# Performance work log

Measured on AMD Instinct MI355X. Metric: run time of the kernel, lower is better.

The kernel has to match this reference:

```python
import jax, jax.numpy as jnp
import numpy as np

N = 16384   # nodes
E = 524288  # edges (avg degree 32)
D = 32      # input_dim == output_dim


def setup_inputs() -> dict:
    key = jax.random.key(0)
    k_x, k_e, k_wa, k_ba, k_wu, k_bu = jax.random.split(key, 6)
    x = jax.random.normal(k_x, (N, D), dtype=jnp.float32)
    edge_index = jax.random.randint(k_e, (2, E), 0, N, dtype=jnp.int32)
    # nn.Linear init: U(-1/sqrt(fan_in), 1/sqrt(fan_in)), weight shape [out, in]
    bound = 1.0 / np.sqrt(D)
    W_agg = jax.random.uniform(k_wa, (D, D), jnp.float32, -bound, bound)
    b_agg = jax.random.uniform(k_ba, (D,), jnp.float32, -bound, bound)
    W_upd = jax.random.uniform(k_wu, (D, D), jnp.float32, -bound, bound)
    b_upd = jax.random.uniform(k_bu, (D,), jnp.float32, -bound, bound)
    return {"x": x, "edge_index": edge_index, "W_agg": W_agg, "b_agg": b_agg,
            "W_upd": W_upd, "b_upd": b_upd}


def reference(x, edge_index, W_agg, b_agg, W_upd, b_upd):
    n = x.shape[0]
    src, dst = edge_index[0], edge_index[1]
    # Dense symmetric 0/1 adjacency, exactly as the torch module builds it
    # (duplicate edges still write 1 via .set, matching index_put semantics).
    adj = jnp.zeros((n, n), dtype=x.dtype)
    adj = adj.at[src, dst].set(1.0)
    adj = adj.at[dst, src].set(1.0)
    messages = adj @ x                              # [N, D]
    aggregated = messages @ W_agg.T + b_agg         # aggregate_fn(messages)
    updated = x @ W_upd.T + b_upd + aggregated      # update_fn(x) + aggregated
    return updated
```

## Files before the change

### kernel.cpp

```cpp
#include <hip/hip_runtime.h>

#define D 32
#define CAP 384


__global__ void gnn_edge_bits(const int* __restrict__ src,
                              const int* __restrict__ dst,
                              unsigned int* __restrict__ bm,
                              int E, int wpr) {
    int e = blockIdx.x * blockDim.x + threadIdx.x;
    if (e >= E) return;
    int s = src[e];
    int d = dst[e];
    atomicOr(&bm[(size_t)d * wpr + (s >> 5)], 1u << (s & 31));
    atomicOr(&bm[(size_t)s * wpr + (d >> 5)], 1u << (d & 31));
}

__global__ __launch_bounds__(256) void gnn_gather_update(
        const unsigned int* __restrict__ bm,
        const float* __restrict__ x,
        float* __restrict__ out,
        const float* __restrict__ W_agg,
        const float* __restrict__ b_agg,
        const float* __restrict__ W_upd,
        const float* __restrict__ b_upd,
        int wpr) {
    __shared__ float sWa[D][D + 1];
    __shared__ float sWu[D][D + 1];
    __shared__ float sb[D];
    __shared__ float sx[4][D];
    __shared__ float sm[4][D];
    __shared__ int   slist[4][CAP];

    int t = threadIdx.x;
    for (int i = t; i < D * D; i += 256) {
        sWa[i >> 5][i & 31] = W_agg[i];
        sWu[i >> 5][i & 31] = W_upd[i];
    }
    if (t < D) sb[t] = b_agg[t] + b_upd[t];

    int lane = t & 63;
    int wv   = t >> 6;
    int dim  = lane & 31;
    int half = lane >> 5;
    size_t node = (size_t)blockIdx.x * 4 + wv;

    if (lane < D) sx[wv][lane] = x[node * D + lane];

    const unsigned int* row = bm + node * (size_t)wpr;
    unsigned int wb[8];
#pragma unroll
    for (int c = 0; c < 8; ++c) wb[c] = row[c * 64 + lane];

    int myc = 0;
#pragma unroll
    for (int c = 0; c < 8; ++c) myc += __popc(wb[c]);

    int pre = myc;
#pragma unroll
    for (int off = 1; off < 64; off <<= 1) {
        int v = __shfl_up(pre, off, 64);
        if (lane >= off) pre += v;
    }
    int total = __shfl(pre, 63, 64);
    pre -= myc;

    if (total <= CAP) {
        int p = pre;
#pragma unroll
        for (int c = 0; c < 8; ++c) {
            unsigned int ww = wb[c];
            int base = (c * 64 + lane) * 32;
            while (ww) {
                int b = __ffs(ww) - 1;
                ww &= ww - 1;
                slist[wv][p++] = base + b;
            }
        }
    }
    __syncthreads();

    float acc = 0.f;
    if (total <= CAP) {
        int j = half;
        for (; j + 8 <= total; j += 8) {
            int c0 = slist[wv][j + 0];
            int c1 = slist[wv][j + 2];
            int c2 = slist[wv][j + 4];
            int c3 = slist[wv][j + 6];
            float v0 = x[(size_t)c0 * D + dim];
            float v1 = x[(size_t)c1 * D + dim];
            float v2 = x[(size_t)c2 * D + dim];
            float v3 = x[(size_t)c3 * D + dim];
            acc += v0; acc += v1; acc += v2; acc += v3;
        }
        for (; j < total; j += 2)
            acc += x[(size_t)slist[wv][j] * D + dim];
        acc += __shfl_xor(acc, 32, 64);
    } else {
        for (int c = 0; c < 8; ++c) {
            unsigned long long m = __ballot(wb[c] != 0);
            while (m) {
                int l = __ffsll(m) - 1;
                m &= m - 1;
                unsigned int ww = __shfl(wb[c], l, 64);
                int basecol = (c * 64 + l) * 32;
                while (ww) {
                    int b = __ffs(ww) - 1;
                    ww &= ww - 1;
                    acc += x[(size_t)(basecol + b) * D + dim];
                }
            }
        }
    }
    if (lane < D) sm[wv][lane] = acc;
    __syncthreads();

    if (t < 128) {
        int ns = t >> 5;
        int o  = t & 31;
        float r = sb[o];
#pragma unroll
        for (int k = 0; k < D; ++k)
            r += sx[ns][k] * sWu[o][k] + sm[ns][k] * sWa[o][k];
        out[((size_t)blockIdx.x * 4 + ns) * D + o] = r;
    }
}

#define HASH_BITS 20
#define HASH_SIZE (1u << HASH_BITS)
#define EMPTY_KEY 0xFFFFFFFFu

__global__ void gnn_edge_scatter(const int* __restrict__ src,
                                 const int* __restrict__ dst,
                                 const float* __restrict__ x,
                                 float* __restrict__ msg,
                                 unsigned int* __restrict__ htab,
                                 int E) {
    int e = blockIdx.x * blockDim.x + threadIdx.x;
    if (e >= E) return;
    int s = src[e];
    int d = dst[e];
    int a = s < d ? s : d;
    int b = s < d ? d : s;
    unsigned int key = ((unsigned int)a << 14) | (unsigned int)b;
    unsigned int h = (key * 2654435761u) >> (32 - HASH_BITS);
    bool inserted;
    for (;;) {
        unsigned int prev = atomicCAS(&htab[h], EMPTY_KEY, key);
        if (prev == EMPTY_KEY) { inserted = true; break; }
        if (prev == key)       { inserted = false; break; }
        h = (h + 1) & (HASH_SIZE - 1);
    }
    if (!inserted) return;
    const float* xs = x + (size_t)s * D;
    const float* xd = x + (size_t)d * D;
    if (s == d) {
        float* mrow = msg + (size_t)s * D;
#pragma unroll
        for (int i = 0; i < D; ++i) atomicAdd(&mrow[i], xs[i]);
    } else {
        float* ms = msg + (size_t)s * D;
        float* md = msg + (size_t)d * D;
#pragma unroll
        for (int i = 0; i < D; ++i) {
            atomicAdd(&ms[i], xd[i]);
            atomicAdd(&md[i], xs[i]);
        }
    }
}

__global__ __launch_bounds__(256) void gnn_update(
        const float* __restrict__ x,
        float* __restrict__ out,
        const float* __restrict__ W_agg,
        const float* __restrict__ b_agg,
        const float* __restrict__ W_upd,
        const float* __restrict__ b_upd) {
    __shared__ float sWa[D][D + 1];
    __shared__ float sWu[D][D + 1];
    __shared__ float sb[D];
    __shared__ float sx[8][D];
    __shared__ float sm[8][D];
    int t = threadIdx.x;
    for (int i = t; i < D * D; i += 256) {
        sWa[i >> 5][i & 31] = W_agg[i];
        sWu[i >> 5][i & 31] = W_upd[i];
    }
    if (t < D) sb[t] = b_agg[t] + b_upd[t];
    int g = t >> 5, o = t & 31;
    size_t node = (size_t)blockIdx.x * 8 + g;
    sx[g][o] = x[node * D + o];
    sm[g][o] = out[node * D + o];
    __syncthreads();
    float acc = sb[o];
#pragma unroll
    for (int k = 0; k < D; ++k) {
        acc += sx[g][k] * sWu[o][k];
        acc += sm[g][k] * sWa[o][k];
    }
    out[node * D + o] = acc;
}


extern "C" void kernel_launch(void* const* d_in, const int* in_sizes, int n_in,
                              void* d_out, int out_size, void* d_ws, size_t ws_size,
                              hipStream_t stream) {
    const float* x      = (const float*)d_in[0];
    const int*   eidx   = (const int*)d_in[1];
    const float* W_agg  = (const float*)d_in[2];
    const float* b_agg  = (const float*)d_in[3];
    const float* W_upd  = (const float*)d_in[4];
    const float* b_upd  = (const float*)d_in[5];
    float* out = (float*)d_out;

    const int E = in_sizes[1] / 2;
    const int N = in_sizes[0] / D;
    const int* src = eidx;
    const int* dst = eidx + E;

    const int wpr = N >> 5;
    const size_t bm_bytes = (size_t)N * wpr * sizeof(unsigned int);

    if (ws_size >= bm_bytes) {
        unsigned int* bm = (unsigned int*)d_ws;
        hipMemsetAsync(bm, 0, bm_bytes, stream);
        gnn_edge_bits<<<(E + 255) / 256, 256, 0, stream>>>(src, dst, bm, E, wpr);
        gnn_gather_update<<<N / 4, 256, 0, stream>>>(bm, x, out, W_agg, b_agg,
                                                     W_upd, b_upd, wpr);
    } else {
        unsigned int* htab = (unsigned int*)d_ws;
        hipMemsetAsync(out, 0, (size_t)N * D * sizeof(float), stream);
        hipMemsetAsync(htab, 0xFF, (size_t)HASH_SIZE * sizeof(unsigned int), stream);
        gnn_edge_scatter<<<(E + 255) / 256, 256, 0, stream>>>(src, dst, x, out, htab, E);
        gnn_update<<<N / 8, 256, 0, stream>>>(x, out, W_agg, b_agg, W_upd, b_upd);
    }
}
```

Before: 134.9 us.

## Replace dense adjacency bitmap with per-node neighbor lists and LDS dedup

Stops building a 32 MB dense adjacency bitmap (memset plus atomicOr) and instead appends each edge endpoint into a fixed-capacity per-node list using padded atomic counters. The gather kernel then reads only the node's list, deduplicates neighbors with a per-wave shared-memory bitmap and atomicOr, compacts the unique indices, and sums x rows. This cuts the memset and the bitmap scan traffic. In exchange it adds contended atomicAdd on counters during build and an overflow fallback that scans all edges for high-degree nodes. The fallback could be very slow if a node's degree ever exceeds the cap.

```diff
diff --git a/kernel.cpp b/kernel.cpp
--- a/kernel.cpp
+++ b/kernel.cpp
@@ -1,36 +1,42 @@
 #include <hip/hip_runtime.h>
 
 #define D 32
-#define CAP 384
-
-
-__global__ void gnn_edge_bits(const int* __restrict__ src,
+#define CAP 256
+#define CSTRIDE 16
+
+__global__ void gnn_csr_build(const int* __restrict__ src,
                               const int* __restrict__ dst,
-                              unsigned int* __restrict__ bm,
-                              int E, int wpr) {
+                              int* __restrict__ cnt,
+                              int* __restrict__ list, int E) {
     int e = blockIdx.x * blockDim.x + threadIdx.x;
     if (e >= E) return;
     int s = src[e];
     int d = dst[e];
-    atomicOr(&bm[(size_t)d * wpr + (s >> 5)], 1u << (s & 31));
-    atomicOr(&bm[(size_t)s * wpr + (d >> 5)], 1u << (d & 31));
+    int p = atomicAdd(&cnt[(size_t)d * CSTRIDE], 1);
+    if (p < CAP) list[(size_t)d * CAP + p] = s;
+    int q = atomicAdd(&cnt[(size_t)s * CSTRIDE], 1);
+    if (q < CAP) list[(size_t)s * CAP + q] = d;
 }
 
 __global__ __launch_bounds__(256) void gnn_gather_update(
-        const unsigned int* __restrict__ bm,
+        const int* __restrict__ cnt,
+        const int* __restrict__ list,
+        const int* __restrict__ src,
+        const int* __restrict__ dst,
+        int E,
         const float* __restrict__ x,
         float* __restrict__ out,
         const float* __restrict__ W_agg,
         const float* __restrict__ b_agg,
         const float* __restrict__ W_upd,
-        const float* __restrict__ b_upd,
-        int wpr) {
+        const float* __restrict__ b_upd) {
     __shared__ float sWa[D][D + 1];
     __shared__ float sWu[D][D + 1];
     __shared__ float sb[D];
     __shared__ float sx[4][D];
     __shared__ float sm[4][D];
-    __shared__ int   slist[4][CAP];
+    __shared__ unsigned int sbit[4][512];
+    __shared__ int slist[4][64];
 
     int t = threadIdx.x;
     for (int i = t; i < D * D; i += 256) {
@@ -47,72 +53,74 @@
 
     if (lane < D) sx[wv][lane] = x[node * D + lane];
 
-    const unsigned int* row = bm + node * (size_t)wpr;
-    unsigned int wb[8];
-#pragma unroll
-    for (int c = 0; c < 8; ++c) wb[c] = row[c * 64 + lane];
-
-    int myc = 0;
-#pragma unroll
-    for (int c = 0; c < 8; ++c) myc += __popc(wb[c]);
-
-    int pre = myc;
-#pragma unroll
-    for (int off = 1; off < 64; off <<= 1) {
-        int v = __shfl_up(pre, off, 64);
-        if (lane >= off) pre += v;
-    }
-    int total = __shfl(pre, 63, 64);
-    pre -= myc;
-
-    if (total <= CAP) {
-        int p = pre;
-#pragma unroll
-        for (int c = 0; c < 8; ++c) {
-            unsigned int ww = wb[c];
-            int base = (c * 64 + lane) * 32;
-            while (ww) {
-                int b = __ffs(ww) - 1;
-                ww &= ww - 1;
-                slist[wv][p++] = base + b;
-            }
+#pragma unroll
+    for (int i = 0; i < 8; ++i) sbit[wv][i * 64 + lane] = 0u;
+
+    int deg = cnt[node * CSTRIDE];
+    float acc = 0.f;
+
+    if (deg <= CAP) {
+        const int* ml = list + node * CAP;
+        for (int base = 0; base < deg; base += 64) {
+            int idx = -1, keep = 0;
+            if (base + lane < deg) {
+                idx = ml[base + lane];
+                unsigned int old = atomicOr(&sbit[wv][idx >> 5], 1u << (idx & 31));
+                keep = !((old >> (idx & 31)) & 1u);
+            }
+            int pre = keep;
+#pragma unroll
+            for (int off = 1; off < 64; off <<= 1) {
+                int v = __shfl_up(pre, off, 64);
+                if (lane >= off) pre += v;
+            }
+            int ckn = __shfl(pre, 63, 64);
+            if (keep) slist[wv][pre - 1] = idx;
+            __asm__ __volatile__("s_waitcnt lgkmcnt(0)" ::: "memory");
+
+            int j = half;
+            for (; j + 8 <= ckn; j += 8) {
+                int c0 = slist[wv][j + 0];
+                int c1 = slist[wv][j + 2];
+                int c2 = slist[wv][j + 4];
+                int c3 = slist[wv][j + 6];
+                float v0 = x[(size_t)c0 * D + dim];
+                float v1 = x[(size_t)c1 * D + dim];
+                float v2 = x[(size_t)c2 * D + dim];
+                float v3 = x[(size_t)c3 * D + dim];
+                acc += v0; acc += v1; acc += v2; acc += v3;
+            }
+            for (; j < ckn; j += 2)
+                acc += x[(size_t)slist[wv][j] * D + dim];
         }
-    }
-    __syncthreads();
-
-    float acc = 0.f;
-    if (total <= CAP) {
-        int j = half;
-        for (; j + 8 <= total; j += 8) {
-            int c0 = slist[wv][j + 0];
-            int c1 = slist[wv][j + 2];
-            int c2 = slist[wv][j + 4];
-            int c3 = slist[wv][j + 6];
-            float v0 = x[(size_t)c0 * D + dim];
-            float v1 = x[(size_t)c1 * D + dim];
-            float v2 = x[(size_t)c2 * D + dim];
-            float v3 = x[(size_t)c3 * D + dim];
-            acc += v0; acc += v1; acc += v2; acc += v3;
+    } else {
+        for (int base = 0; base < E; base += 64) {
+            int e = base + lane;
+            int nbr = -1, keep = 0;
+            if (e < E) {
+                int s = src[e], d = dst[e];
+                if (s == (int)node)      nbr = d;
+                else if (d == (int)node) nbr = s;
+            }
+            if (nbr >= 0) {
+                unsigned int old = atomicOr(&sbit[wv][nbr >> 5], 1u << (nbr & 31));
+                keep = !((old >> (nbr & 31)) & 1u);
+            }
+            int pre = keep;
+#pragma unroll
+            for (int off = 1; off < 64; off <<= 1) {
+                int v = __shfl_up(pre, off, 64);
+                if (lane >= off) pre += v;
+            }
+            int ckn = __shfl(pre, 63, 64);
+            if (keep) slist[wv][pre - 1] = nbr;
+            __asm__ __volatile__("s_waitcnt lgkmcnt(0)" ::: "memory");
+            for (int j = half; j < ckn; j += 2)
+                acc += x[(size_t)slist[wv][j] * D + dim];
         }
-        for (; j < total; j += 2)
-            acc += x[(size_t)slist[wv][j] * D + dim];
-        acc += __shfl_xor(acc, 32, 64);
-    } else {
-        for (int c = 0; c < 8; ++c) {
-            unsigned long long m = __ballot(wb[c] != 0);
-            while (m) {
-                int l = __ffsll(m) - 1;
-                m &= m - 1;
-                unsigned int ww = __shfl(wb[c], l, 64);
-                int basecol = (c * 64 + l) * 32;
-                while (ww) {
-                    int b = __ffs(ww) - 1;
-                    ww &= ww - 1;
-                    acc += x[(size_t)(basecol + b) * D + dim];
-                }
-            }
-        }
-    }
+    }
+
+    acc += __shfl_xor(acc, 32, 64);
     if (lane < D) sm[wv][lane] = acc;
     __syncthreads();
 
@@ -219,15 +227,17 @@
     const int* src = eidx;
     const int* dst = eidx + E;
 
-    const int wpr = N >> 5;
-    const size_t bm_bytes = (size_t)N * wpr * sizeof(unsigned int);
-
-    if (ws_size >= bm_bytes) {
-        unsigned int* bm = (unsigned int*)d_ws;
-        hipMemsetAsync(bm, 0, bm_bytes, stream);
-        gnn_edge_bits<<<(E + 255) / 256, 256, 0, stream>>>(src, dst, bm, E, wpr);
-        gnn_gather_update<<<N / 4, 256, 0, stream>>>(bm, x, out, W_agg, b_agg,
-                                                     W_upd, b_upd, wpr);
+    const size_t cnt_bytes  = (size_t)N * CSTRIDE * sizeof(int);
+    const size_t list_bytes = (size_t)N * CAP * sizeof(int);
+
+    if (ws_size >= cnt_bytes + list_bytes) {
+        int* cnt  = (int*)d_ws;
+        int* list = (int*)((char*)d_ws + cnt_bytes);
+        hipMemsetAsync(cnt, 0, cnt_bytes, stream);
+        gnn_csr_build<<<(E + 255) / 256, 256, 0, stream>>>(src, dst, cnt, list, E);
+        gnn_gather_update<<<N / 4, 256, 0, stream>>>(cnt, list, src, dst, E,
+                                                     x, out, W_agg, b_agg,
+                                                     W_upd, b_upd);
     } else {
         unsigned int* htab = (unsigned int*)d_ws;
         hipMemsetAsync(out, 0, (size_t)N * D * sizeof(float), stream);
```

Result: slower. 153.2 us (+13.5%).

## Replace global adjacency bitmap with two-level edge binning and per-block shared bitmaps

Applied to the files above, without the earlier changes.

Drops the 32 MB global bitmap (memset plus scattered atomicOr plus full-row reads) in favour of two binning passes that bucket packed edge entries by destination node group into global lists. Each gather block then builds a 16-node bitmap in shared memory for deduplication, and gathers and applies the linear layers for those 16 nodes. This cuts global memory traffic, at the cost of two extra kernels, spill-buffer handling and much larger shared memory per block. The hash fallback key is also changed to be N-based.

```diff
diff --git a/kernel.cpp b/kernel.cpp
--- a/kernel.cpp
+++ b/kernel.cpp
@@ -1,129 +1,208 @@
 #include <hip/hip_runtime.h>
 
 #define D 32
-#define CAP 384
-
-
-__global__ void gnn_edge_bits(const int* __restrict__ src,
-                              const int* __restrict__ dst,
-                              unsigned int* __restrict__ bm,
-                              int E, int wpr) {
-    int e = blockIdx.x * blockDim.x + threadIdx.x;
-    if (e >= E) return;
-    int s = src[e];
-    int d = dst[e];
-    atomicOr(&bm[(size_t)d * wpr + (s >> 5)], 1u << (s & 31));
-    atomicOr(&bm[(size_t)s * wpr + (d >> 5)], 1u << (d & 31));
+
+#define NB_C     8
+#define FPERC    128
+#define NB_F     1024
+#define CCAP     524288
+#define FCAP     4096
+#define SPILLCAP 8192
+#define A_EPB    4096
+#define A_CAP    512
+#define A2_EPB   8192
+#define A2_CAP   128
+#define GCAP     256
+
+__global__ __launch_bounds__(256) void gnn_bin_coarse(
+        const int* __restrict__ src, const int* __restrict__ dst, int E,
+        unsigned int* __restrict__ clist, int* __restrict__ ccnt,
+        unsigned int* __restrict__ spill, int* __restrict__ spillcnt) {
+    __shared__ unsigned int buf[4][NB_C][A_CAP];
+    __shared__ int bcnt[4][NB_C];
+    int t = threadIdx.x, wv = t >> 6, lane = t & 63;
+    if (lane < NB_C) bcnt[wv][lane] = 0;
+    __syncthreads();
+
+    int base = blockIdx.x * A_EPB;
+    int lim  = min(base + A_EPB, E);
+    for (int e = base + t; e < lim; e += 256) {
+        int s = src[e], d2 = dst[e];
+        unsigned int e1 = ((unsigned int)d2 << 14) | (unsigned int)s;
+        unsigned int e2 = ((unsigned int)s  << 14) | (unsigned int)d2;
+        int b1 = d2 >> 11, b2 = s >> 11;
+        int p1 = atomicAdd(&bcnt[wv][b1], 1);
+        if (p1 < A_CAP) buf[wv][b1][p1] = e1;
+        else { int sp = atomicAdd(spillcnt, 1); if (sp < SPILLCAP) spill[sp] = e1; }
+        int p2 = atomicAdd(&bcnt[wv][b2], 1);
+        if (p2 < A_CAP) buf[wv][b2][p2] = e2;
+        else { int sp = atomicAdd(spillcnt, 1); if (sp < SPILLCAP) spill[sp] = e2; }
+    }
+    __syncthreads();
+
+    for (int b = 0; b < NB_C; ++b) {
+        int c = bcnt[wv][b]; if (c > A_CAP) c = A_CAP;
+        if (c == 0) continue;
+        int gbase = 0;
+        if (lane == 0) gbase = atomicAdd(&ccnt[b], c);
+        gbase = __shfl(gbase, 0, 64);
+        for (int i = lane; i < c; i += 64) {
+            int pos = gbase + i;
+            unsigned int v = buf[wv][b][i];
+            if (pos < CCAP) clist[(size_t)b * CCAP + pos] = v;
+            else { int sp = atomicAdd(spillcnt, 1); if (sp < SPILLCAP) spill[sp] = v; }
+        }
+    }
+}
+
+__global__ __launch_bounds__(256) void gnn_bin_fine(
+        const unsigned int* __restrict__ clist, const int* __restrict__ ccnt,
+        unsigned int* __restrict__ flist, int* __restrict__ fcnt,
+        unsigned int* __restrict__ spill, int* __restrict__ spillcnt) {
+    int cb = blockIdx.x & (NB_C - 1);
+    int slice = blockIdx.x >> 3;
+    int cnt = ccnt[cb]; if (cnt > CCAP) cnt = CCAP;
+    int base = slice * A2_EPB;
+    if (base >= cnt) return;
+    int lim = min(base + A2_EPB, cnt);
+
+    __shared__ unsigned int buf[FPERC][A2_CAP];
+    __shared__ int bcnt[FPERC];
+    int t = threadIdx.x;
+    if (t < FPERC) bcnt[t] = 0;
+    __syncthreads();
+
+    const unsigned int* cl = clist + (size_t)cb * CCAP;
+    for (int i = base + t; i < lim; i += 256) {
+        unsigned int en = cl[i];
+        int fb = (en >> 18) & (FPERC - 1);
+        int p = atomicAdd(&bcnt[fb], 1);
+        if (p < A2_CAP) buf[fb][p] = en;
+        else { int sp = atomicAdd(spillcnt, 1); if (sp < SPILLCAP) spill[sp] = en; }
+    }
+    __syncthreads();
+
+    if (t < FPERC) {
+        int c = bcnt[t]; if (c > A2_CAP) c = A2_CAP;
+        if (c) {
+            int fg = cb * FPERC + t;
+            int g = atomicAdd(&fcnt[fg], c);
+            unsigned int* fl = flist + (size_t)fg * FCAP;
+            for (int i = 0; i < c; ++i) {
+                int pos = g + i;
+                unsigned int v = buf[t][i];
+                if (pos < FCAP) fl[pos] = v;
+                else { int sp = atomicAdd(spillcnt, 1); if (sp < SPILLCAP) spill[sp] = v; }
+            }
+        }
+    }
 }
 
 __global__ __launch_bounds__(256) void gnn_gather_update(
-        const unsigned int* __restrict__ bm,
-        const float* __restrict__ x,
-        float* __restrict__ out,
-        const float* __restrict__ W_agg,
-        const float* __restrict__ b_agg,
-        const float* __restrict__ W_upd,
-        const float* __restrict__ b_upd,
-        int wpr) {
-    __shared__ float sWa[D][D + 1];
-    __shared__ float sWu[D][D + 1];
-    __shared__ float sb[D];
-    __shared__ float sx[4][D];
-    __shared__ float sm[4][D];
-    __shared__ int   slist[4][CAP];
+        const unsigned int* __restrict__ flist, const int* __restrict__ fcnt,
+        const unsigned int* __restrict__ spill, const int* __restrict__ spillcnt,
+        const float* __restrict__ x, float* __restrict__ out,
+        const float* __restrict__ W_agg, const float* __restrict__ b_agg,
+        const float* __restrict__ W_upd, const float* __restrict__ b_upd) {
+    __shared__ unsigned int sbit[16][512];
+    __shared__ float sWa[D][D + 1], sWu[D][D + 1];
+    __shared__ float sbias[D];
+    __shared__ float sxn[16][D], smsg[16][D];
+    __shared__ int slist[4][GCAP];
 
     int t = threadIdx.x;
+    int fb = blockIdx.x;
+
+    for (int i = t; i < 16 * 512; i += 256) ((unsigned int*)sbit)[i] = 0u;
     for (int i = t; i < D * D; i += 256) {
         sWa[i >> 5][i & 31] = W_agg[i];
         sWu[i >> 5][i & 31] = W_upd[i];
     }
-    if (t < D) sb[t] = b_agg[t] + b_upd[t];
-
-    int lane = t & 63;
-    int wv   = t >> 6;
-    int dim  = lane & 31;
-    int half = lane >> 5;
-    size_t node = (size_t)blockIdx.x * 4 + wv;
-
-    if (lane < D) sx[wv][lane] = x[node * D + lane];
-
-    const unsigned int* row = bm + node * (size_t)wpr;
-    unsigned int wb[8];
-#pragma unroll
-    for (int c = 0; c < 8; ++c) wb[c] = row[c * 64 + lane];
-
-    int myc = 0;
-#pragma unroll
-    for (int c = 0; c < 8; ++c) myc += __popc(wb[c]);
-
-    int pre = myc;
-#pragma unroll
-    for (int off = 1; off < 64; off <<= 1) {
-        int v = __shfl_up(pre, off, 64);
-        if (lane >= off) pre += v;
-    }
-    int total = __shfl(pre, 63, 64);
-    pre -= myc;
-
-    if (total <= CAP) {
-        int p = pre;
-#pragma unroll
-        for (int c = 0; c < 8; ++c) {
-            unsigned int ww = wb[c];
-            int base = (c * 64 + lane) * 32;
-            while (ww) {
-                int b = __ffs(ww) - 1;
-                ww &= ww - 1;
-                slist[wv][p++] = base + b;
+    if (t < D) sbias[t] = b_agg[t] + b_upd[t];
+    for (int i = t; i < 16 * D; i += 256)
+        ((float*)sxn)[i] = x[(size_t)fb * 16 * D + i];
+    __syncthreads();
+
+    int cnt = fcnt[fb]; if (cnt > FCAP) cnt = FCAP;
+    const unsigned int* fl = flist + (size_t)fb * FCAP;
+    for (int i = t; i < cnt; i += 256) {
+        unsigned int en = fl[i];
+        int nl = (en >> 14) & 15;
+        int nbr = en & 16383;
+        atomicOr(&sbit[nl][nbr >> 5], 1u << (nbr & 31));
+    }
+    int sc = *spillcnt; if (sc > SPILLCAP) sc = SPILLCAP;
+    for (int i = t; i < sc; i += 256) {
+        unsigned int en = spill[i];
+        int node = en >> 14;
+        if ((node >> 4) == fb) {
+            int nbr = en & 16383;
+            atomicOr(&sbit[node & 15][nbr >> 5], 1u << (nbr & 31));
+        }
+    }
+    __syncthreads();
+
+    int wv = t >> 6, lane = t & 63, dim = lane & 31, half = lane >> 5;
+    for (int q = 0; q < 4; ++q) {
+        int nl = wv * 4 + q;
+        unsigned int w[8];
+#pragma unroll
+        for (int c = 0; c < 8; ++c) w[c] = sbit[nl][c * 64 + lane];
+        int myc = 0;
+#pragma unroll
+        for (int c = 0; c < 8; ++c) myc += __popc(w[c]);
+        int pre = myc;
+#pragma unroll
+        for (int off = 1; off < 64; off <<= 1) {
+            int v = __shfl_up(pre, off, 64);
+            if (lane >= off) pre += v;
+        }
+        int total = __shfl(pre, 63, 64);
+        pre -= myc;
+        float acc = 0.f;
+        if (total <= GCAP) {
+            int p = pre;
+#pragma unroll
+            for (int c = 0; c < 8; ++c) {
+                unsigned int ww = w[c];
+                int bb = (c * 64 + lane) * 32;
+                while (ww) { int b = __ffs(ww) - 1; ww &= ww - 1; slist[wv][p++] = bb + b; }
             }
-        }
-    }
-    __syncthreads();
-
-    float acc = 0.f;
-    if (total <= CAP) {
-        int j = half;
-        for (; j + 8 <= total; j += 8) {
-            int c0 = slist[wv][j + 0];
-            int c1 = slist[wv][j + 2];
-            int c2 = slist[wv][j + 4];
-            int c3 = slist[wv][j + 6];
-            float v0 = x[(size_t)c0 * D + dim];
-            float v1 = x[(size_t)c1 * D + dim];
-            float v2 = x[(size_t)c2 * D + dim];
-            float v3 = x[(size_t)c3 * D + dim];
-            acc += v0; acc += v1; acc += v2; acc += v3;
-        }
-        for (; j < total; j += 2)
-            acc += x[(size_t)slist[wv][j] * D + dim];
-        acc += __shfl_xor(acc, 32, 64);
-    } else {
-        for (int c = 0; c < 8; ++c) {
-            unsigned long long m = __ballot(wb[c] != 0);
-            while (m) {
-                int l = __ffsll(m) - 1;
-                m &= m - 1;
-                unsigned int ww = __shfl(wb[c], l, 64);
-                int basecol = (c * 64 + l) * 32;
-                while (ww) {
-                    int b = __ffs(ww) - 1;
-                    ww &= ww - 1;
-                    acc += x[(size_t)(basecol + b) * D + dim];
+            int j = half;
+            for (; j + 8 <= total; j += 8) {
+                int c0 = slist[wv][j + 0], c1 = slist[wv][j + 2];
+                int c2 = slist[wv][j + 4], c3 = slist[wv][j + 6];
+                float v0 = x[(size_t)c0 * D + dim];
+                float v1 = x[(size_t)c1 * D + dim];
+                float v2 = x[(size_t)c2 * D + dim];
+                float v3 = x[(size_t)c3 * D + dim];
+                acc += v0; acc += v1; acc += v2; acc += v3;
+            }
+            for (; j < total; j += 2) acc += x[(size_t)slist[wv][j] * D + dim];
+        } else {
+            for (int c = 0; c < 8; ++c) {
+                unsigned long long m = __ballot(w[c] != 0);
+                while (m) {
+                    int l = __ffsll(m) - 1; m &= m - 1;
+                    unsigned int ww = __shfl(w[c], l, 64);
+                    int bb = (c * 64 + l) * 32;
+                    while (ww) { int b = __ffs(ww) - 1; ww &= ww - 1;
+                                 acc += x[(size_t)(bb + b) * D + dim]; }
                 }
             }
         }
-    }
-    if (lane < D) sm[wv][lane] = acc;
-    __syncthreads();
-
-    if (t < 128) {
-        int ns = t >> 5;
-        int o  = t & 31;
-        float r = sb[o];
+        acc += __shfl_xor(acc, 32, 64);
+        if (lane < D) smsg[nl][lane] = acc;
+    }
+    __syncthreads();
+
+    for (int o = t; o < 16 * D; o += 256) {
+        int nl = o >> 5, od = o & 31;
+        float r = sbias[od];
 #pragma unroll
         for (int k = 0; k < D; ++k)
-            r += sx[ns][k] * sWu[o][k] + sm[ns][k] * sWa[o][k];
-        out[((size_t)blockIdx.x * 4 + ns) * D + o] = r;
+            r += sxn[nl][k] * sWu[od][k] + smsg[nl][k] * sWa[od][k];
+        out[((size_t)fb * 16 + nl) * D + od] = r;
     }
 }
 
@@ -135,30 +214,28 @@
                                  const int* __restrict__ dst,
                                  const float* __restrict__ x,
                                  float* __restrict__ msg,
-                                 unsigned int* __restrict__ htab,
-                                 int E) {
+                                 unsigned int* __restrict__ htab, int E, int N) {
     int e = blockIdx.x * blockDim.x + threadIdx.x;
     if (e >= E) return;
-    int s = src[e];
-    int d = dst[e];
-    int a = s < d ? s : d;
-    int b = s < d ? d : s;
-    unsigned int key = ((unsigned int)a << 14) | (unsigned int)b;
-    unsigned int h = (key * 2654435761u) >> (32 - HASH_BITS);
+    int s = src[e], d = dst[e];
+    int a = s < d ? s : d, b = s < d ? d : s;
+    unsigned long long key = (unsigned long long)a * N + b;
+    unsigned int k32 = (unsigned int)(key & 0xFFFFFFFEu) | 1u;
+    unsigned int h = ((unsigned int)key * 2654435761u) >> (32 - HASH_BITS);
     bool inserted;
     for (;;) {
-        unsigned int prev = atomicCAS(&htab[h], EMPTY_KEY, key);
+        unsigned int prev = atomicCAS(&htab[h], EMPTY_KEY, k32);
         if (prev == EMPTY_KEY) { inserted = true; break; }
-        if (prev == key)       { inserted = false; break; }
+        if (prev == k32)       { inserted = false; break; }
         h = (h + 1) & (HASH_SIZE - 1);
     }
     if (!inserted) return;
     const float* xs = x + (size_t)s * D;
     const float* xd = x + (size_t)d * D;
     if (s == d) {
-        float* mrow = msg + (size_t)s * D;
-#pragma unroll
-        for (int i = 0; i < D; ++i) atomicAdd(&mrow[i], xs[i]);
+        float* m = msg + (size_t)s * D;
+#pragma unroll
+        for (int i = 0; i < D; ++i) atomicAdd(&m[i], xs[i]);
     } else {
         float* ms = msg + (size_t)s * D;
         float* md = msg + (size_t)d * D;
@@ -171,17 +248,11 @@
 }
 
 __global__ __launch_bounds__(256) void gnn_update(
-        const float* __restrict__ x,
-        float* __restrict__ out,
-        const float* __restrict__ W_agg,
-        const float* __restrict__ b_agg,
-        const float* __restrict__ W_upd,
-        const float* __restrict__ b_upd) {
-    __shared__ float sWa[D][D + 1];
-    __shared__ float sWu[D][D + 1];
-    __shared__ float sb[D];
-    __shared__ float sx[8][D];
-    __shared__ float sm[8][D];
+        const float* __restrict__ x, float* __restrict__ out,
+        const float* __restrict__ W_agg, const float* __restrict__ b_agg,
+        const float* __restrict__ W_upd, const float* __restrict__ b_upd) {
+    __shared__ float sWa[D][D + 1], sWu[D][D + 1], sb[D];
+    __shared__ float sx[8][D], sm[8][D];
     int t = threadIdx.x;
     for (int i = t; i < D * D; i += 256) {
         sWa[i >> 5][i & 31] = W_agg[i];
@@ -195,10 +266,8 @@
     __syncthreads();
     float acc = sb[o];
 #pragma unroll
-    for (int k = 0; k < D; ++k) {
-        acc += sx[g][k] * sWu[o][k];
-        acc += sm[g][k] * sWa[o][k];
-    }
+    for (int k = 0; k < D; ++k)
+        acc += sx[g][k] * sWu[o][k] + sm[g][k] * sWa[o][k];
     out[node * D + o] = acc;
 }
 
@@ -206,12 +275,12 @@
 extern "C" void kernel_launch(void* const* d_in, const int* in_sizes, int n_in,
                               void* d_out, int out_size, void* d_ws, size_t ws_size,
                               hipStream_t stream) {
-    const float* x      = (const float*)d_in[0];
-    const int*   eidx   = (const int*)d_in[1];
-    const float* W_agg  = (const float*)d_in[2];
-    const float* b_agg  = (const float*)d_in[3];
-    const float* W_upd  = (const float*)d_in[4];
-    const float* b_upd  = (const float*)d_in[5];
+    const float* x     = (const float*)d_in[0];
+    const int*   eidx  = (const int*)d_in[1];
+    const float* W_agg = (const float*)d_in[2];
+    const float* b_agg = (const float*)d_in[3];
+    const float* W_upd = (const float*)d_in[4];
+    const float* b_upd = (const float*)d_in[5];
     float* out = (float*)d_out;
 
     const int E = in_sizes[1] / 2;
@@ -219,20 +288,30 @@
     const int* src = eidx;
     const int* dst = eidx + E;
 
-    const int wpr = N >> 5;
-    const size_t bm_bytes = (size_t)N * wpr * sizeof(unsigned int);
-
-    if (ws_size >= bm_bytes) {
-        unsigned int* bm = (unsigned int*)d_ws;
-        hipMemsetAsync(bm, 0, bm_bytes, stream);
-        gnn_edge_bits<<<(E + 255) / 256, 256, 0, stream>>>(src, dst, bm, E, wpr);
-        gnn_gather_update<<<N / 4, 256, 0, stream>>>(bm, x, out, W_agg, b_agg,
-                                                     W_upd, b_upd, wpr);
+    char* w = (char*)d_ws;
+    int* ccnt = (int*)w;
+    int* fcnt = (int*)(w + 64);
+    int* spillcnt = (int*)(w + 4160);
+    unsigned int* clist = (unsigned int*)(w + 8192);
+    unsigned int* flist = clist + (size_t)NB_C * CCAP;
+    unsigned int* spill = flist + (size_t)NB_F * FCAP;
+    size_t need = 8192 + (size_t)NB_C * CCAP * 4 + (size_t)NB_F * FCAP * 4
+                + (size_t)SPILLCAP * 4;
+
+    if (N == 16384 && ws_size >= need) {
+        hipMemsetAsync(w, 0, 8192, stream);
+        gnn_bin_coarse<<<(E + A_EPB - 1) / A_EPB, 256, 0, stream>>>(
+            src, dst, E, clist, ccnt, spill, spillcnt);
+        gnn_bin_fine<<<NB_C * 64, 256, 0, stream>>>(
+            clist, ccnt, flist, fcnt, spill, spillcnt);
+        gnn_gather_update<<<NB_F, 256, 0, stream>>>(
+            flist, fcnt, spill, spillcnt, x, out, W_agg, b_agg, W_upd, b_upd);
     } else {
         unsigned int* htab = (unsigned int*)d_ws;
         hipMemsetAsync(out, 0, (size_t)N * D * sizeof(float), stream);
         hipMemsetAsync(htab, 0xFF, (size_t)HASH_SIZE * sizeof(unsigned int), stream);
-        gnn_edge_scatter<<<(E + 255) / 256, 256, 0, stream>>>(src, dst, x, out, htab, E);
+        gnn_edge_scatter<<<(E + 255) / 256, 256, 0, stream>>>(src, dst, x, out,
+                                                              htab, E, N);
         gnn_update<<<N / 8, 256, 0, stream>>>(x, out, W_agg, b_agg, W_upd, b_upd);
     }
 }
```

After: 183.2 us. +35.8%, slower.

## Process four nodes per wavefront with vectorized bitmap row loads

Applied to the files above, without the earlier changes.

The gather kernel now handles 16 nodes per block (4 per wavefront) instead of 4. Each lane loads bitmap rows as uint4, and the per-wave column list is built and consumed without a block-wide barrier. The gather loop is unrolled to 8 outstanding loads, and the weight-matrix setup is amortized over more nodes. The list cap shrinks to 256, and the fallback hash path changes its key encoding. This raises register pressure and lowers the block count, which may reduce occupancy.

```diff
diff --git a/kernel.cpp b/kernel.cpp
--- a/kernel.cpp
+++ b/kernel.cpp
@@ -1,8 +1,7 @@
 #include <hip/hip_runtime.h>
 
 #define D 32
-#define CAP 384
-
+#define GCAP 256
 
 __global__ void gnn_edge_bits(const int* __restrict__ src,
                               const int* __restrict__ dst,
@@ -27,103 +26,120 @@
         int wpr) {
     __shared__ float sWa[D][D + 1];
     __shared__ float sWu[D][D + 1];
-    __shared__ float sb[D];
-    __shared__ float sx[4][D];
-    __shared__ float sm[4][D];
-    __shared__ int   slist[4][CAP];
+    __shared__ float sbias[D];
+    __shared__ float sx[16][D];
+    __shared__ float sm[16][D];
+    __shared__ int   slist[4][4][GCAP];
 
     int t = threadIdx.x;
     for (int i = t; i < D * D; i += 256) {
         sWa[i >> 5][i & 31] = W_agg[i];
         sWu[i >> 5][i & 31] = W_upd[i];
     }
-    if (t < D) sb[t] = b_agg[t] + b_upd[t];
+    if (t < D) sbias[t] = b_agg[t] + b_upd[t];
+    for (int i = t; i < 16 * D; i += 256)
+        ((float*)sx)[i] = x[(size_t)blockIdx.x * 16 * D + i];
 
     int lane = t & 63;
     int wv   = t >> 6;
     int dim  = lane & 31;
     int half = lane >> 5;
-    size_t node = (size_t)blockIdx.x * 4 + wv;
-
-    if (lane < D) sx[wv][lane] = x[node * D + lane];
-
-    const unsigned int* row = bm + node * (size_t)wpr;
-    unsigned int wb[8];
-#pragma unroll
-    for (int c = 0; c < 8; ++c) wb[c] = row[c * 64 + lane];
-
-    int myc = 0;
-#pragma unroll
-    for (int c = 0; c < 8; ++c) myc += __popc(wb[c]);
-
-    int pre = myc;
-#pragma unroll
-    for (int off = 1; off < 64; off <<= 1) {
-        int v = __shfl_up(pre, off, 64);
-        if (lane >= off) pre += v;
-    }
-    int total = __shfl(pre, 63, 64);
-    pre -= myc;
-
-    if (total <= CAP) {
-        int p = pre;
-#pragma unroll
-        for (int c = 0; c < 8; ++c) {
-            unsigned int ww = wb[c];
-            int base = (c * 64 + lane) * 32;
-            while (ww) {
-                int b = __ffs(ww) - 1;
-                ww &= ww - 1;
-                slist[wv][p++] = base + b;
-            }
+    int nb   = blockIdx.x * 16 + wv * 4;
+
+    uint4 q[8];
+#pragma unroll
+    for (int nn = 0; nn < 4; ++nn) {
+        const uint4* row = (const uint4*)(bm + (size_t)(nb + nn) * wpr);
+        q[nn * 2 + 0] = row[lane];
+        q[nn * 2 + 1] = row[64 + lane];
+    }
+
+    float accs[4];
+#pragma unroll
+    for (int nn = 0; nn < 4; ++nn) {
+        unsigned int w[8] = { q[nn*2].x,   q[nn*2].y,   q[nn*2].z,   q[nn*2].w,
+                              q[nn*2+1].x, q[nn*2+1].y, q[nn*2+1].z, q[nn*2+1].w };
+        int myc = 0;
+#pragma unroll
+        for (int k = 0; k < 8; ++k) myc += __popc(w[k]);
+        int pre = myc;
+#pragma unroll
+        for (int off = 1; off < 64; off <<= 1) {
+            int v = __shfl_up(pre, off, 64);
+            if (lane >= off) pre += v;
         }
-    }
-    __syncthreads();
-
-    float acc = 0.f;
-    if (total <= CAP) {
-        int j = half;
-        for (; j + 8 <= total; j += 8) {
-            int c0 = slist[wv][j + 0];
-            int c1 = slist[wv][j + 2];
-            int c2 = slist[wv][j + 4];
-            int c3 = slist[wv][j + 6];
-            float v0 = x[(size_t)c0 * D + dim];
-            float v1 = x[(size_t)c1 * D + dim];
-            float v2 = x[(size_t)c2 * D + dim];
-            float v3 = x[(size_t)c3 * D + dim];
-            acc += v0; acc += v1; acc += v2; acc += v3;
-        }
-        for (; j < total; j += 2)
-            acc += x[(size_t)slist[wv][j] * D + dim];
-        acc += __shfl_xor(acc, 32, 64);
-    } else {
-        for (int c = 0; c < 8; ++c) {
-            unsigned long long m = __ballot(wb[c] != 0);
-            while (m) {
-                int l = __ffsll(m) - 1;
-                m &= m - 1;
-                unsigned int ww = __shfl(wb[c], l, 64);
-                int basecol = (c * 64 + l) * 32;
+        int total = __shfl(pre, 63, 64);
+        pre -= myc;
+
+        float acc = 0.f;
+        if (total <= GCAP) {
+            int p = pre;
+#pragma unroll
+            for (int k = 0; k < 8; ++k) {
+                unsigned int ww = w[k];
+                int widx = (k < 4) ? (4 * lane + k) : (256 + 4 * lane + k - 4);
+                int base = widx * 32;
                 while (ww) {
                     int b = __ffs(ww) - 1;
                     ww &= ww - 1;
-                    acc += x[(size_t)(basecol + b) * D + dim];
+                    slist[wv][nn][p++] = base + b;
+                }
+            }
+            __asm__ __volatile__("s_waitcnt lgkmcnt(0)" ::: "memory");
+
+            const int* sl = slist[wv][nn];
+            int j = half;
+            for (; j + 16 <= total; j += 16) {
+                int c0 = sl[j +  0], c1 = sl[j +  2], c2 = sl[j +  4], c3 = sl[j +  6];
+                int c4 = sl[j +  8], c5 = sl[j + 10], c6 = sl[j + 12], c7 = sl[j + 14];
+                float v0 = x[(size_t)c0 * D + dim];
+                float v1 = x[(size_t)c1 * D + dim];
+                float v2 = x[(size_t)c2 * D + dim];
+                float v3 = x[(size_t)c3 * D + dim];
+                float v4 = x[(size_t)c4 * D + dim];
+                float v5 = x[(size_t)c5 * D + dim];
+                float v6 = x[(size_t)c6 * D + dim];
+                float v7 = x[(size_t)c7 * D + dim];
+                acc += v0; acc += v1; acc += v2; acc += v3;
+                acc += v4; acc += v5; acc += v6; acc += v7;
+            }
+            for (; j < total; j += 2)
+                acc += x[(size_t)sl[j] * D + dim];
+        } else {
+#pragma unroll
+            for (int k = 0; k < 8; ++k) {
+                unsigned long long m = __ballot(w[k] != 0);
+                while (m) {
+                    int l = __ffsll(m) - 1;
+                    m &= m - 1;
+                    unsigned int ww = __shfl(w[k], l, 64);
+                    int widx = (k < 4) ? (4 * l + k) : (256 + 4 * l + k - 4);
+                    int base = widx * 32;
+                    while (ww) {
+                        int b = __ffs(ww) - 1;
+                        ww &= ww - 1;
+                        acc += x[(size_t)(base + b) * D + dim];
+                    }
                 }
             }
         }
-    }
-    if (lane < D) sm[wv][lane] = acc;
+        accs[nn] = acc;
+    }
+
+#pragma unroll
+    for (int nn = 0; nn < 4; ++nn) {
+        float a = accs[nn] + __shfl_xor(accs[nn], 32, 64);
+        if (lane < D) sm[wv * 4 + nn][lane] = a;
+    }
     __syncthreads();
 
-    if (t < 128) {
-        int ns = t >> 5;
-        int o  = t & 31;
-        float r = sb[o];
+    for (int o = t; o < 16 * D; o += 256) {
+        int nl = o >> 5, od = o & 31;
+        float r = sbias[od];
 #pragma unroll
         for (int k = 0; k < D; ++k)
-            r += sx[ns][k] * sWu[o][k] + sm[ns][k] * sWa[o][k];
-        out[((size_t)blockIdx.x * 4 + ns) * D + o] = r;
+            r += sx[nl][k] * sWu[od][k] + sm[nl][k] * sWa[od][k];
+        out[((size_t)blockIdx.x * 16 + nl) * D + od] = r;
     }
 }
 
@@ -135,30 +151,28 @@
                                  const int* __restrict__ dst,
                                  const float* __restrict__ x,
                                  float* __restrict__ msg,
-                                 unsigned int* __restrict__ htab,
-                                 int E) {
+                                 unsigned int* __restrict__ htab, int E, int N) {
     int e = blockIdx.x * blockDim.x + threadIdx.x;
     if (e >= E) return;
-    int s = src[e];
-    int d = dst[e];
-    int a = s < d ? s : d;
-    int b = s < d ? d : s;
-    unsigned int key = ((unsigned int)a << 14) | (unsigned int)b;
-    unsigned int h = (key * 2654435761u) >> (32 - HASH_BITS);
+    int s = src[e], d = dst[e];
+    int a = s < d ? s : d, b = s < d ? d : s;
+    unsigned long long key = (unsigned long long)a * N + b;
+    unsigned int k32 = (unsigned int)(key & 0xFFFFFFFEu) | 1u;
+    unsigned int h = ((unsigned int)key * 2654435761u) >> (32 - HASH_BITS);
     bool inserted;
     for (;;) {
-        unsigned int prev = atomicCAS(&htab[h], EMPTY_KEY, key);
+        unsigned int prev = atomicCAS(&htab[h], EMPTY_KEY, k32);
         if (prev == EMPTY_KEY) { inserted = true; break; }
-        if (prev == key)       { inserted = false; break; }
+        if (prev == k32)       { inserted = false; break; }
         h = (h + 1) & (HASH_SIZE - 1);
     }
     if (!inserted) return;
     const float* xs = x + (size_t)s * D;
     const float* xd = x + (size_t)d * D;
     if (s == d) {
-        float* mrow = msg + (size_t)s * D;
-#pragma unroll
-        for (int i = 0; i < D; ++i) atomicAdd(&mrow[i], xs[i]);
+        float* m = msg + (size_t)s * D;
+#pragma unroll
+        for (int i = 0; i < D; ++i) atomicAdd(&m[i], xs[i]);
     } else {
         float* ms = msg + (size_t)s * D;
         float* md = msg + (size_t)d * D;
@@ -171,17 +185,11 @@
 }
 
 __global__ __launch_bounds__(256) void gnn_update(
-        const float* __restrict__ x,
-        float* __restrict__ out,
-        const float* __restrict__ W_agg,
-        const float* __restrict__ b_agg,
-        const float* __restrict__ W_upd,
-        const float* __restrict__ b_upd) {
-    __shared__ float sWa[D][D + 1];
-    __shared__ float sWu[D][D + 1];
-    __shared__ float sb[D];
-    __shared__ float sx[8][D];
-    __shared__ float sm[8][D];
+        const float* __restrict__ x, float* __restrict__ out,
+        const float* __restrict__ W_agg, const float* __restrict__ b_agg,
+        const float* __restrict__ W_upd, const float* __restrict__ b_upd) {
+    __shared__ float sWa[D][D + 1], sWu[D][D + 1], sb[D];
+    __shared__ float sx[8][D], sm[8][D];
     int t = threadIdx.x;
     for (int i = t; i < D * D; i += 256) {
         sWa[i >> 5][i & 31] = W_agg[i];
@@ -195,10 +203,8 @@
     __syncthreads();
     float acc = sb[o];
 #pragma unroll
-    for (int k = 0; k < D; ++k) {
-        acc += sx[g][k] * sWu[o][k];
-        acc += sm[g][k] * sWa[o][k];
-    }
+    for (int k = 0; k < D; ++k)
+        acc += sx[g][k] * sWu[o][k] + sm[g][k] * sWa[o][k];
     out[node * D + o] = acc;
 }
 
@@ -206,12 +212,12 @@
 extern "C" void kernel_launch(void* const* d_in, const int* in_sizes, int n_in,
                               void* d_out, int out_size, void* d_ws, size_t ws_size,
                               hipStream_t stream) {
-    const float* x      = (const float*)d_in[0];
-    const int*   eidx   = (const int*)d_in[1];
-    const float* W_agg  = (const float*)d_in[2];
-    const float* b_agg  = (const float*)d_in[3];
-    const float* W_upd  = (const float*)d_in[4];
-    const float* b_upd  = (const float*)d_in[5];
+    const float* x     = (const float*)d_in[0];
+    const int*   eidx  = (const int*)d_in[1];
+    const float* W_agg = (const float*)d_in[2];
+    const float* b_agg = (const float*)d_in[3];
+    const float* W_upd = (const float*)d_in[4];
+    const float* b_upd = (const float*)d_in[5];
     float* out = (float*)d_out;
 
     const int E = in_sizes[1] / 2;
@@ -222,17 +228,18 @@
     const int wpr = N >> 5;
     const size_t bm_bytes = (size_t)N * wpr * sizeof(unsigned int);
 
-    if (ws_size >= bm_bytes) {
+    if ((N & 15) == 0 && ws_size >= bm_bytes) {
         unsigned int* bm = (unsigned int*)d_ws;
         hipMemsetAsync(bm, 0, bm_bytes, stream);
         gnn_edge_bits<<<(E + 255) / 256, 256, 0, stream>>>(src, dst, bm, E, wpr);
-        gnn_gather_update<<<N / 4, 256, 0, stream>>>(bm, x, out, W_agg, b_agg,
-                                                     W_upd, b_upd, wpr);
+        gnn_gather_update<<<N / 16, 256, 0, stream>>>(bm, x, out, W_agg, b_agg,
+                                                      W_upd, b_upd, wpr);
     } else {
         unsigned int* htab = (unsigned int*)d_ws;
         hipMemsetAsync(out, 0, (size_t)N * D * sizeof(float), stream);
         hipMemsetAsync(htab, 0xFF, (size_t)HASH_SIZE * sizeof(unsigned int), stream);
-        gnn_edge_scatter<<<(E + 255) / 256, 256, 0, stream>>>(src, dst, x, out, htab, E);
+        gnn_edge_scatter<<<(E + 255) / 256, 256, 0, stream>>>(src, dst, x, out,
+                                                              htab, E, N);
         gnn_update<<<N / 8, 256, 0, stream>>>(x, out, W_agg, b_agg, W_upd, b_upd);
     }
 }
```

After: 147.2 us. +9.1%, slower.
